# Optimization experiments

Hardware: AMD Instinct MI355X
Metric: run time of the kernel (lower is better)

The kernel has to match this reference:

```python
import jax, jax.numpy as jnp
import numpy as np

B, F, D, K, H, W = 8, 16, 256, 3, 64, 64

def setup_inputs() -> dict:
    key = jax.random.key(0)
    k1, k2, k3, k4 = jax.random.split(key, 4)
    return {
        "x": jax.random.normal(k1, (B, D, H, W), dtype=jnp.float32),
        "bank_request": jax.random.normal(k2, (B, F), dtype=jnp.float32),
        "style": jax.random.normal(k3, (B, 1, D, 1, 1), dtype=jnp.float32),
        "bank_weight": jax.random.normal(k4, (F, D, D, K, K), dtype=jnp.float32),
    }

def reference(x, bank_request, style, bank_weight):
    # softmax-weighted filter bank sum -> per-sample kernel (b, o, i, kh, kw)
    w = jax.nn.softmax(bank_request, axis=1)                      # (b, f)
    kernel = jnp.einsum('bf,foihw->boihw', w, bank_weight)
    # style modulation
    kernel = kernel * (1.0 + style)
    # L2 demodulation over (i, kh, kw)
    norm = jax.lax.rsqrt(jnp.sum(kernel * kernel, axis=(2, 3, 4), keepdims=True) + 1e-8)
    kernel = kernel * norm
    # per-sample conv2d, stride 1, SAME padding (odd symmetric kernel)
    def conv_one(xi, ki):
        return jax.lax.conv_general_dilated(
            xi[None], ki, window_strides=(1, 1), padding='SAME',
            dimension_numbers=('NCHW', 'OIHW', 'NCHW'))[0]
    return jax.vmap(conv_one)(x, kernel)
```

## Files before the change

kernel.cpp:

```cpp
#include <hip/hip_runtime.h>
#include <hip/hip_bf16.h>
#include <math.h>

#define BB 8
#define FF 16
#define DD 256
#define HH 64
#define WW 64

typedef short bf16x8 __attribute__((ext_vector_type(8)));
typedef float f32x4 __attribute__((ext_vector_type(4)));

__device__ inline ushort f2bf(float f) {
    union { float f; unsigned u; } v; v.f = f;
    unsigned r = v.u + 0x7FFFu + ((v.u >> 16) & 1u);
    return (ushort)(r >> 16);
}

__global__ __launch_bounds__(256) void cast_x(
    const float* __restrict__ x,
    ushort* __restrict__ xb)
{
    __shared__ ushort ls[64][258];
    const int r = blockIdx.x, b = blockIdx.y, t = threadIdx.x;

    const int c4 = (t & 15) * 4;
    const int ig = t >> 4;
#pragma unroll
    for (int j = 0; j < 16; ++j) {
        const int i = ig * 16 + j;
        const float4 xv = *reinterpret_cast<const float4*>(
            x + (((size_t)(b * DD + i) * HH) + r) * WW + c4);
        ls[c4 + 0][i] = f2bf(xv.x);
        ls[c4 + 1][i] = f2bf(xv.y);
        ls[c4 + 2][i] = f2bf(xv.z);
        ls[c4 + 3][i] = f2bf(xv.w);
    }
    __syncthreads();

    const int i2 = t & 127;
    const int ch = t >> 7;
#pragma unroll
    for (int cl = 0; cl < 32; ++cl) {
        const int c = ch * 32 + cl;
        const unsigned u = (unsigned)ls[c][2 * i2] | ((unsigned)ls[c][2 * i2 + 1] << 16);
        *reinterpret_cast<unsigned*>(xb + (((size_t)(b * HH + r) * WW) + c) * DD + 2 * i2) = u;
    }
}

__global__ __launch_bounds__(256) void prep_filter(
    const float* __restrict__ bank_request,
    const float* __restrict__ style,
    const float* __restrict__ bank_weight,
    ushort* __restrict__ Ak)
{
    const int o = blockIdx.x;
    const int i = threadIdx.x;

    __shared__ float wsm[BB][FF];
    __shared__ float red[4][BB];
    __shared__ float nrm[BB];

    if (i < BB) {
        float v[FF];
        float m = -1e30f;
#pragma unroll
        for (int f = 0; f < FF; ++f) {
            v[f] = bank_request[i * FF + f];
            m = fmaxf(m, v[f]);
        }
        float s = 0.f;
#pragma unroll
        for (int f = 0; f < FF; ++f) { v[f] = __expf(v[f] - m); s += v[f]; }
        const float inv = 1.0f / s;
#pragma unroll
        for (int f = 0; f < FF; ++f) wsm[i][f] = v[f] * inv;
    }
    __syncthreads();

    float acc9[BB][9];
#pragma unroll
    for (int b = 0; b < BB; ++b)
#pragma unroll
        for (int j = 0; j < 9; ++j) acc9[b][j] = 0.f;

    float pre[2][9];
#pragma unroll
    for (int s = 0; s < 2; ++s) {
        const float* p = bank_weight + ((size_t)(s * DD + o) * DD + i) * 9;
#pragma unroll
        for (int j = 0; j < 9; ++j) pre[s][j] = p[j];
    }
#pragma unroll
    for (int f = 0; f < FF; ++f) {
        const int sl = f & 1;
        float cur[9];
#pragma unroll
        for (int j = 0; j < 9; ++j) cur[j] = pre[sl][j];
        if (f + 2 < FF) {
            const float* p = bank_weight + ((size_t)((f + 2) * DD + o) * DD + i) * 9;
#pragma unroll
            for (int j = 0; j < 9; ++j) pre[sl][j] = p[j];
        }
#pragma unroll
        for (int b = 0; b < BB; ++b) {
            const float wf = wsm[b][f];
#pragma unroll
            for (int j = 0; j < 9; ++j) acc9[b][j] = fmaf(wf, cur[j], acc9[b][j]);
        }
    }

    float ss[BB];
#pragma unroll
    for (int b = 0; b < BB; ++b) {
        const float sm = 1.0f + style[b * DD + i];
        float t = 0.f;
#pragma unroll
        for (int j = 0; j < 9; ++j) {
            acc9[b][j] *= sm;
            t = fmaf(acc9[b][j], acc9[b][j], t);
        }
        ss[b] = t;
    }

    const int wave = i >> 6, lane = i & 63;
#pragma unroll
    for (int b = 0; b < BB; ++b) {
        float tv = ss[b];
#pragma unroll
        for (int off = 32; off > 0; off >>= 1) tv += __shfl_down(tv, off, 64);
        if (lane == 0) red[wave][b] = tv;
    }
    __syncthreads();
    if (i < BB)
        nrm[i] = rsqrtf(red[0][i] + red[1][i] + red[2][i] + red[3][i] + 1e-8f);
    __syncthreads();

    const int ib = i >> 3, e = i & 7;
#pragma unroll
    for (int b = 0; b < BB; ++b) {
        const float nb = nrm[b];
#pragma unroll
        for (int j = 0; j < 9; ++j) {
            const size_t idx = ((((size_t)(b * 9 + j) * 32 + ib) * DD) + o) * 8 + e;
            Ak[idx] = f2bf(acc9[b][j] * nb);
        }
    }
}

#define XROWS 6
#define XCELLS 66
#define XCELLB 80
#define XBUF (XROWS * XCELLS * XCELLB)

__global__ __launch_bounds__(512, 2) void conv_mfma(
    const ushort* __restrict__ xb,
    const ushort* __restrict__ Ak,
    float* __restrict__ out)
{
    __shared__ __align__(16) char xs[2 * XBUF];

    const int rg = blockIdx.x, ot = blockIdx.y, b = blockIdx.z;
    const int r0 = rg * 4, o0 = ot * 128;
    const int t = threadIdx.x;
    const int w = t >> 6, l = t & 63;
    const int wm = w >> 2;
    const int wn = w & 3;
    const int lo = l & 15, lhi = l >> 4;

    const ushort* sg_ptr[4];
    int sg_lds[4];
    bool sg_ok[4];
    bool sg_act[4];
#pragma unroll
    for (int s = 0; s < 4; ++s) {
        const int idx = t + s * 512;
        sg_act[s] = idx < XROWS * XCELLS * 4;
        const int row = idx / (XCELLS * 4);
        const int rem = idx - row * (XCELLS * 4);
        const int cell = rem >> 2;
        const int q = rem & 3;
        const int gr = r0 - 1 + row;
        const int gc = cell - 1;
        sg_ok[s] = sg_act[s] && ((unsigned)gr < 64u) && ((unsigned)gc < 64u);
        sg_ptr[s] = xb + (((size_t)(b * HH + (gr & 63)) * WW) + (gc & 63)) * DD + q * 8;
        sg_lds[s] = (row * XCELLS + cell) * XCELLB + q * 16;
    }

    f32x4 acc[4][4];
#pragma unroll
    for (int a = 0; a < 4; ++a)
#pragma unroll
        for (int c = 0; c < 4; ++c)
#pragma unroll
            for (int j = 0; j < 4; ++j) acc[a][c][j] = 0.f;

    const int obase = o0 + wm * 64 + lo;
    const int bLane = lo * XCELLB + lhi * 16;

    bf16x8 vr[4];
    bf16x8 aF[3][4], bF[2][4];

#define LDA(tp, sl, aB)  do {                                                  \
        const ushort* ap_ = (aB) + (size_t)(tp) * 65536;                       \
        aF[sl][0] = *reinterpret_cast<const bf16x8*>(ap_);                     \
        aF[sl][1] = *reinterpret_cast<const bf16x8*>(ap_ + 128);               \
        aF[sl][2] = *reinterpret_cast<const bf16x8*>(ap_ + 256);               \
        aF[sl][3] = *reinterpret_cast<const bf16x8*>(ap_ + 384);               \
    } while (0)

#define LDB(tp, sl, bufc)  do {                                                \
        const int dr_ = (tp) / 3, dc_ = (tp) % 3;                              \
        const char* bb_ = (bufc) + ((wn + dr_) * XCELLS + dc_) * XCELLB;       \
        bF[sl][0] = *reinterpret_cast<const bf16x8*>(bb_);                     \
        bF[sl][1] = *reinterpret_cast<const bf16x8*>(bb_ + 16 * XCELLB);       \
        bF[sl][2] = *reinterpret_cast<const bf16x8*>(bb_ + 32 * XCELLB);       \
        bF[sl][3] = *reinterpret_cast<const bf16x8*>(bb_ + 48 * XCELLB);       \
    } while (0)

#pragma unroll
    for (int s = 0; s < 4; ++s) {
        bf16x8 v = {0, 0, 0, 0, 0, 0, 0, 0};
        if (sg_ok[s]) v = *reinterpret_cast<const bf16x8*>(sg_ptr[s]);
        vr[s] = v;
    }
#pragma unroll
    for (int s = 0; s < 4; ++s)
        if (sg_act[s]) *reinterpret_cast<bf16x8*>(xs + sg_lds[s]) = vr[s];
    __syncthreads();

    for (int kc = 0; kc < 8; ++kc) {
        const int cur = kc & 1;

        if (kc < 7) {
            const int ioff = (kc + 1) * 32;
#pragma unroll
            for (int s = 0; s < 4; ++s) {
                bf16x8 v = {0, 0, 0, 0, 0, 0, 0, 0};
                if (sg_ok[s]) v = *reinterpret_cast<const bf16x8*>(sg_ptr[s] + ioff);
                vr[s] = v;
            }
        }

        const char* bufc = xs + cur * XBUF + bLane;
        const int ib = kc * 4 + lhi;
        const ushort* aBase = Ak + (((size_t)b * 9 * 32 + ib) * DD + obase) * 8;

        LDA(0, 0, aBase);
        LDA(1, 1, aBase);
        LDB(0, 0, bufc);
#pragma unroll
        for (int tap = 0; tap < 9; ++tap) {
            const int as = tap % 3;
            if (tap + 2 <= 8) LDA(tap + 2, (tap + 2) % 3, aBase);
            if (tap < 8) LDB(tap + 1, (tap + 1) & 1, bufc);
            const int bs = tap & 1;
            __builtin_amdgcn_s_setprio(1);
#pragma unroll
            for (int fm = 0; fm < 4; ++fm)
#pragma unroll
                for (int fn = 0; fn < 4; ++fn)
                    acc[fm][fn] = __builtin_amdgcn_mfma_f32_16x16x32_bf16(
                        aF[as][fm], bF[bs][fn], acc[fm][fn], 0, 0, 0);
            __builtin_amdgcn_s_setprio(0);
        }

        if (kc < 7) {
            char* dstb = xs + (cur ^ 1) * XBUF;
#pragma unroll
            for (int s = 0; s < 4; ++s)
                if (sg_act[s]) *reinterpret_cast<bf16x8*>(dstb + sg_lds[s]) = vr[s];
        }
        __syncthreads();
    }
#undef LDA
#undef LDB

    const int r_out = r0 + wn;
#pragma unroll
    for (int fm = 0; fm < 4; ++fm) {
#pragma unroll
        for (int fn = 0; fn < 4; ++fn) {
            const int oo = o0 + wm * 64 + fm * 16 + lhi * 4;
            const int cc = fn * 16 + lo;
            float* op = out + (((size_t)(b * DD + oo) * HH) + r_out) * WW + cc;
#pragma unroll
            for (int j = 0; j < 4; ++j) op[(size_t)j * HH * WW] = acc[fm][fn][j];
        }
    }
}

extern "C" void kernel_launch(void* const* d_in, const int* in_sizes, int n_in,
                              void* d_out, int out_size, void* d_ws, size_t ws_size,
                              hipStream_t stream) {
    const float* x            = (const float*)d_in[0];
    const float* bank_request = (const float*)d_in[1];
    const float* style        = (const float*)d_in[2];
    const float* bank_weight  = (const float*)d_in[3];
    float* out = (float*)d_out;

    ushort* Ak = (ushort*)d_ws;
    ushort* xb = Ak + (size_t)8 * 9 * 32 * 256 * 8;

    cast_x<<<dim3(HH, BB), 256, 0, stream>>>(x, xb);
    prep_filter<<<dim3(DD), 256, 0, stream>>>(bank_request, style, bank_weight, Ak);
    conv_mfma<<<dim3(16, 2, BB), 512, 0, stream>>>(xb, Ak, out);
}
```

Before: 66.46 us.

## Halve conv row tile, raise occupancy, and remap blocks across XCDs

The conv kernel now computes 2 output rows per block instead of 4. Each wave covers half the columns with 4x2 MFMA tiles, and the LDS halo buffer drops from 6 to 4 rows. This doubles the grid to 512 blocks, cuts per-block LDS and registers, and lets launch bounds ask for 4 blocks per CU. A 1D grid decoding places blocks of the same batch and output-channel group on the same XCD for L2 reuse of filters. In exchange the halo re-read overhead per output row rises and the MFMA work per B-fragment load shrinks.

```diff
diff --git a/kernel.cpp b/kernel.cpp
--- a/kernel.cpp
+++ b/kernel.cpp
@@ -148,58 +148,66 @@
     }
 }
 
-#define XROWS 6
+#define XROWS 4
 #define XCELLS 66
 #define XCELLB 80
 #define XBUF (XROWS * XCELLS * XCELLB)
 
-__global__ __launch_bounds__(512, 2) void conv_mfma(
+__global__ __launch_bounds__(512, 4) void conv_mfma(
     const ushort* __restrict__ xb,
     const ushort* __restrict__ Ak,
     float* __restrict__ out)
 {
     __shared__ __align__(16) char xs[2 * XBUF];
 
-    const int rg = blockIdx.x, ot = blockIdx.y, b = blockIdx.z;
-    const int r0 = rg * 4, o0 = ot * 128;
+    const int wg = blockIdx.x;
+    const int xcd = wg & 7;
+    const int rem = wg >> 3;
+    const int rg = rem & 31;
+    const int Ghi = rem >> 5;
+    const int G = xcd + 8 * Ghi;
+    const int ot = G & 1, b = G >> 1;
+
+    const int r0 = rg * 2, o0 = ot * 128;
     const int t = threadIdx.x;
     const int w = t >> 6, l = t & 63;
     const int wm = w >> 2;
-    const int wn = w & 3;
+    const int wn = (w >> 1) & 1;
+    const int wp = w & 1;
     const int lo = l & 15, lhi = l >> 4;
 
-    const ushort* sg_ptr[4];
-    int sg_lds[4];
-    bool sg_ok[4];
-    bool sg_act[4];
-#pragma unroll
-    for (int s = 0; s < 4; ++s) {
+    const ushort* sg_ptr[3];
+    int sg_lds[3];
+    bool sg_ok[3];
+#pragma unroll
+    for (int s = 0; s < 3; ++s) {
         const int idx = t + s * 512;
-        sg_act[s] = idx < XROWS * XCELLS * 4;
+        const bool active = (s < 2) || (t < 32);
         const int row = idx / (XCELLS * 4);
-        const int rem = idx - row * (XCELLS * 4);
-        const int cell = rem >> 2;
-        const int q = rem & 3;
+        const int rem2 = idx - row * (XCELLS * 4);
+        const int cell = rem2 >> 2;
+        const int q = rem2 & 3;
         const int gr = r0 - 1 + row;
         const int gc = cell - 1;
-        sg_ok[s] = sg_act[s] && ((unsigned)gr < 64u) && ((unsigned)gc < 64u);
+        sg_ok[s] = active && ((unsigned)gr < 64u) && ((unsigned)gc < 64u);
         sg_ptr[s] = xb + (((size_t)(b * HH + (gr & 63)) * WW) + (gc & 63)) * DD + q * 8;
         sg_lds[s] = (row * XCELLS + cell) * XCELLB + q * 16;
     }
-
-    f32x4 acc[4][4];
+    const bool sg_act2 = (t < 32);
+
+    f32x4 acc[4][2];
 #pragma unroll
     for (int a = 0; a < 4; ++a)
 #pragma unroll
-        for (int c = 0; c < 4; ++c)
+        for (int c = 0; c < 2; ++c)
 #pragma unroll
             for (int j = 0; j < 4; ++j) acc[a][c][j] = 0.f;
 
     const int obase = o0 + wm * 64 + lo;
-    const int bLane = lo * XCELLB + lhi * 16;
-
-    bf16x8 vr[4];
-    bf16x8 aF[3][4], bF[2][4];
+    const int bLane = (wp * 32 + lo) * XCELLB + lhi * 16;
+
+    bf16x8 vr[3];
+    bf16x8 aF[3][4], bF[2][2];
 
 #define LDA(tp, sl, aB)  do {                                                  \
         const ushort* ap_ = (aB) + (size_t)(tp) * 65536;                       \
@@ -214,19 +222,16 @@
         const char* bb_ = (bufc) + ((wn + dr_) * XCELLS + dc_) * XCELLB;       \
         bF[sl][0] = *reinterpret_cast<const bf16x8*>(bb_);                     \
         bF[sl][1] = *reinterpret_cast<const bf16x8*>(bb_ + 16 * XCELLB);       \
-        bF[sl][2] = *reinterpret_cast<const bf16x8*>(bb_ + 32 * XCELLB);       \
-        bF[sl][3] = *reinterpret_cast<const bf16x8*>(bb_ + 48 * XCELLB);       \
     } while (0)
 
 #pragma unroll
-    for (int s = 0; s < 4; ++s) {
-        bf16x8 v = {0, 0, 0, 0, 0, 0, 0, 0};
-        if (sg_ok[s]) v = *reinterpret_cast<const bf16x8*>(sg_ptr[s]);
-        vr[s] = v;
-    }
-#pragma unroll
-    for (int s = 0; s < 4; ++s)
-        if (sg_act[s]) *reinterpret_cast<bf16x8*>(xs + sg_lds[s]) = vr[s];
+    for (int s = 0; s < 3; ++s) {
+        if (s < 2 || sg_act2) {
+            bf16x8 v = {0, 0, 0, 0, 0, 0, 0, 0};
+            if (sg_ok[s]) v = *reinterpret_cast<const bf16x8*>(sg_ptr[s]);
+            *reinterpret_cast<bf16x8*>(xs + sg_lds[s]) = v;
+        }
+    }
     __syncthreads();
 
     for (int kc = 0; kc < 8; ++kc) {
@@ -235,7 +240,7 @@
         if (kc < 7) {
             const int ioff = (kc + 1) * 32;
 #pragma unroll
-            for (int s = 0; s < 4; ++s) {
+            for (int s = 0; s < 3; ++s) {
                 bf16x8 v = {0, 0, 0, 0, 0, 0, 0, 0};
                 if (sg_ok[s]) v = *reinterpret_cast<const bf16x8*>(sg_ptr[s] + ioff);
                 vr[s] = v;
@@ -259,7 +264,7 @@
 #pragma unroll
             for (int fm = 0; fm < 4; ++fm)
 #pragma unroll
-                for (int fn = 0; fn < 4; ++fn)
+                for (int fn = 0; fn < 2; ++fn)
                     acc[fm][fn] = __builtin_amdgcn_mfma_f32_16x16x32_bf16(
                         aF[as][fm], bF[bs][fn], acc[fm][fn], 0, 0, 0);
             __builtin_amdgcn_s_setprio(0);
@@ -268,8 +273,9 @@
         if (kc < 7) {
             char* dstb = xs + (cur ^ 1) * XBUF;
 #pragma unroll
-            for (int s = 0; s < 4; ++s)
-                if (sg_act[s]) *reinterpret_cast<bf16x8*>(dstb + sg_lds[s]) = vr[s];
+            for (int s = 0; s < 3; ++s)
+                if (s < 2 || sg_act2)
+                    *reinterpret_cast<bf16x8*>(dstb + sg_lds[s]) = vr[s];
         }
         __syncthreads();
     }
@@ -280,9 +286,9 @@
 #pragma unroll
     for (int fm = 0; fm < 4; ++fm) {
 #pragma unroll
-        for (int fn = 0; fn < 4; ++fn) {
+        for (int fn = 0; fn < 2; ++fn) {
             const int oo = o0 + wm * 64 + fm * 16 + lhi * 4;
-            const int cc = fn * 16 + lo;
+            const int cc = wp * 32 + fn * 16 + lo;
             float* op = out + (((size_t)(b * DD + oo) * HH) + r_out) * WW + cc;
 #pragma unroll
             for (int j = 0; j < 4; ++j) op[(size_t)j * HH * WW] = acc[fm][fn][j];
@@ -304,5 +310,5 @@
 
     cast_x<<<dim3(HH, BB), 256, 0, stream>>>(x, xb);
     prep_filter<<<dim3(DD), 256, 0, stream>>>(bank_request, style, bank_weight, Ak);
-    conv_mfma<<<dim3(16, 2, BB), 512, 0, stream>>>(xb, Ak, out);
-}
+    conv_mfma<<<dim3(512), 512, 0, stream>>>(xb, Ak, out);
+}
```

New measurement: 77.08 us. +16.0%, slower.
